# Optimization experiments

Hardware: AMD Instinct MI355X
Metric: run time of the kernel (lower is better)

Reference implementation:

```python
import jax, jax.numpy as jnp
import numpy as np

N, F, D, C, K, E, M = 50000, 512, 128, 128, 3, 20000, 8  # nodes, feat, emb, conv, cheb K, hyperedges, edge size
EPS = 1e-5


def setup_inputs() -> dict:
    key = jax.random.key(0)
    ks = jax.random.split(key, 9)
    pos_set = jax.random.normal(ks[0], (N, F), jnp.float32)
    # each hyperedge = M distinct nodes (contiguous window => distinct, like the original expansion assumes)
    base = jax.random.randint(ks[1], (E, 1), 0, N - M)
    members = (base + jnp.arange(M, dtype=jnp.int32)[None, :]).astype(jnp.int32)  # [E, M]
    # expansion(): full directed clique (no self loops) on the E*M duplicated entries
    row, col = np.where(~np.eye(M, dtype=bool))            # M*(M-1) intra-edge pairs
    offs = np.arange(E, dtype=np.int64)[:, None] * M
    edge_index = jnp.asarray(np.stack([(offs + row[None, :]).ravel(),
                                       (offs + col[None, :]).ravel()]), jnp.int32)  # [2, E*M*(M-1)]
    batch = jnp.asarray(np.repeat(np.arange(E, dtype=np.int64), M), jnp.int32)      # [E*M]
    W_enc = jax.random.normal(ks[2], (F, D), jnp.float32) / np.float32(np.sqrt(F))
    b_enc = jnp.zeros((D,), jnp.float32)
    gn_gamma = 1.0 + 0.1 * jax.random.normal(ks[3], (D,), jnp.float32)
    gn_beta = 0.01 * jax.random.normal(ks[4], (D,), jnp.float32)
    gn_alpha = 1.0 + 0.1 * jax.random.normal(ks[5], (D,), jnp.float32)
    cheb_W = jax.random.normal(ks[6], (K, D, C), jnp.float32) / np.float32(np.sqrt(D * K))
    cheb_b = jnp.zeros((C,), jnp.float32)
    lin_W = jax.random.normal(ks[7], (2 * C, 1), jnp.float32) / np.float32(np.sqrt(2 * C))
    lin_b = jnp.zeros((1,), jnp.float32)
    return dict(pos_set=pos_set, W_enc=W_enc, b_enc=b_enc, gn_gamma=gn_gamma, gn_beta=gn_beta,
                gn_alpha=gn_alpha, cheb_W=cheb_W, cheb_b=cheb_b, lin_W=lin_W, lin_b=lin_b,
                members=members, edge_index=edge_index, batch=batch)


def reference(pos_set, W_enc, b_enc, gn_gamma, gn_beta, gn_alpha, cheb_W, cheb_b,
              lin_W, lin_b, members, edge_index, batch):
    num_entries = E * M
    # running_type == 'structure': Hardtanh(Linear(feature))
    x = jnp.clip(pos_set @ W_enc + b_enc, -1.0, 1.0)                    # [N, D]
    # partition(): duplicate node features per (node, hyperedge) incidence
    xe = x[members.reshape(-1)]                                         # [E*M, D]
    # GraphNorm (per-hyperedge group): out = gamma*(x - alpha*mean)/sqrt(var+eps) + beta
    cnt = jax.ops.segment_sum(jnp.ones((num_entries,), xe.dtype), batch, num_segments=E)  # [E]
    mean = jax.ops.segment_sum(xe, batch, num_segments=E) / cnt[:, None]
    ctr = xe - gn_alpha * mean[batch]
    var = jax.ops.segment_sum(ctr * ctr, batch, num_segments=E) / cnt[:, None]
    xe = gn_gamma * ctr / jnp.sqrt(var + EPS)[batch] + gn_beta
    # AlphaDropout is identity at eval time
    # ChebConv: sym norm, lambda_max=2 => L_hat = -D^{-1/2} A D^{-1/2} (zero diagonal)
    src, dst = edge_index[0], edge_index[1]
    deg = jax.ops.segment_sum(jnp.ones_like(src, dtype=xe.dtype), dst, num_segments=num_entries)
    w = -jax.lax.rsqrt(deg[src] * deg[dst])                             # [nE] scaled-Laplacian weights

    def Lhat(h):  # sparse matvec via gather + segment scatter-add
        return jax.ops.segment_sum(w[:, None] * h[src], dst, num_segments=num_entries)

    Tx0 = xe
    Tx1 = Lhat(Tx0)
    out = Tx0 @ cheb_W[0] + Tx1 @ cheb_W[1]
    Tkm1, Tkm2 = Tx1, Tx0
    for k in range(2, K):  # K is a small static constant
        Tk = 2.0 * Lhat(Tkm1) - Tkm2
        out = out + Tk @ cheb_W[k]
        Tkm1, Tkm2 = Tk, Tkm1
    h = jnp.clip(out + cheb_b, -1.0, 1.0)                               # Hardtanh
    # poolings per hyperedge
    y_max = jax.ops.segment_max(h, batch, num_segments=E)
    y_min = jax.ops.segment_min(h, batch, num_segments=E)
    y_norm = jnp.sqrt(jax.ops.segment_sum(h * h, batch, num_segments=E) / cnt[:, None])
    y = jnp.concatenate([y_max - y_min, y_norm], axis=1)                # [E, 2C]
    logits = y @ lin_W + lin_b
    return jax.nn.sigmoid(logits).squeeze(-1)                           # [E] link probabilities
```

## Files before the change

### kernel.cpp

```cpp
#include <hip/hip_runtime.h>
#include <hip/hip_bf16.h>

#define NN   50000
#define FF   512
#define DD   128
#define CC   128
#define EE   20000
#define MM   8
#define EPSV 1e-5f

typedef __attribute__((ext_vector_type(8)))  short bfrag;
typedef __attribute__((ext_vector_type(16))) float f32x16;

#define MFMA32(a, b, c) __builtin_amdgcn_mfma_f32_32x32x16_bf16((a), (b), (c), 0, 0, 0)

__device__ __forceinline__ unsigned short f2bf(float f) {
    unsigned u = __builtin_bit_cast(unsigned, f);
    unsigned r = u + 0x7FFFu + ((u >> 16) & 1u);
    return (unsigned short)(r >> 16);
}
__device__ __forceinline__ float bf2f(unsigned short h) {
    unsigned u = ((unsigned)h) << 16;
    return __builtin_bit_cast(float, u);
}
__device__ __forceinline__ void split1(float a, short& hi, short& lo) {
    unsigned short h = f2bf(a);
    hi = (short)h;
    lo = (short)f2bf(a - bf2f(h));
}

__global__ void prep_kernel(const float* __restrict__ W_enc,
                            const float* __restrict__ cheb_W,
                            unsigned short* __restrict__ WencT_hi,
                            unsigned short* __restrict__ WencT_lo,
                            unsigned short* __restrict__ WabT_hi,
                            unsigned short* __restrict__ WabT_lo) {
    int tid = blockIdx.x * blockDim.x + threadIdx.x;
    int stride = gridDim.x * blockDim.x;
    for (int idx = tid; idx < DD * FF; idx += stride) {
        int n = idx / FF, k = idx % FF;
        float v = W_enc[k * DD + n];
        short hi, lo; split1(v, hi, lo);
        WencT_hi[idx] = (unsigned short)hi;
        WencT_lo[idx] = (unsigned short)lo;
    }
    const float c1 = 1.0f / 7.0f;
    const float c2 = -47.0f / 49.0f;
    const float c3 = -1.0f / 7.0f;
    const float c4 = 12.0f / 49.0f;
    for (int idx = tid; idx < DD * 256; idx += stride) {
        int c = idx / 256, k = idx % 256;
        float v;
        if (k < DD) {
            v = cheb_W[0 * DD * CC + k * CC + c]
              + c1 * cheb_W[1 * DD * CC + k * CC + c]
              + c2 * cheb_W[2 * DD * CC + k * CC + c];
        } else {
            int d = k - DD;
            v = c3 * cheb_W[1 * DD * CC + d * CC + c]
              + c4 * cheb_W[2 * DD * CC + d * CC + c];
        }
        short hi, lo; split1(v, hi, lo);
        WabT_hi[idx] = (unsigned short)hi;
        WabT_lo[idx] = (unsigned short)lo;
    }
}

__global__ __launch_bounds__(512, 6) void enc_kernel(
        const float* __restrict__ pos,
        const unsigned short* __restrict__ BT_hi,
        const unsigned short* __restrict__ BT_lo,
        const float* __restrict__ b_enc,
        float* __restrict__ x) {
    __shared__ unsigned short ahz[2][64 * 64];
    __shared__ unsigned short bhz[2][128 * 64];

    const int t = threadIdx.x;
    const int w = t >> 6, l = t & 63, l31 = l & 31, lg2 = l >> 5;
    const int wm = w & 1, wn = w >> 1;

    f32x16 acc;
#pragma unroll
    for (int i = 0; i < 16; i++) acc[i] = 0.f;

    for (int ph = 0; ph < 8; ph++) {
        if (ph) __syncthreads();
        {
            const int r = t >> 3, c8 = t & 7;
            int grow = blockIdx.x * 64 + r;
            if (grow >= NN) grow = NN - 1;
            const float* src = pos + (size_t)grow * FF + ph * 64 + c8 * 8;
            const float4 v0 = *(const float4*)src;
            const float4 v1 = *(const float4*)(src + 4);
            const float av[8] = {v0.x, v0.y, v0.z, v0.w, v1.x, v1.y, v1.z, v1.w};
            bfrag hi, lo;
#pragma unroll
            for (int j = 0; j < 8; j++) { short h, lo2; split1(av[j], h, lo2); hi[j] = h; lo[j] = lo2; }
            const int dst = r * 64 + ((c8 ^ (r & 7)) << 3);
            *(bfrag*)&ahz[0][dst] = hi;
            *(bfrag*)&ahz[1][dst] = lo;
        }
#pragma unroll
        for (int i = 0; i < 4; i++) {
            const int c = t + i * 512;
            const int arr = c >> 10, rc = c & 1023, n = rc >> 3, slot = rc & 7;
            const unsigned short* src = (arr ? BT_lo : BT_hi) + (size_t)n * FF + ph * 64 + slot * 8;
            *(bfrag*)&bhz[arr][n * 64 + ((slot ^ (n & 7)) << 3)] = *(const bfrag*)src;
        }
        __syncthreads();
#pragma unroll
        for (int ks = 0; ks < 4; ks++) {
            const int slot = ks * 2 + lg2;
            const int arow = wm * 32 + l31;
            const int aoff = arow * 64 + ((slot ^ (arow & 7)) << 3);
            const bfrag ahi = *(const bfrag*)&ahz[0][aoff];
            const bfrag alo = *(const bfrag*)&ahz[1][aoff];
            const int col = wn * 32 + l31;
            const int boff = col * 64 + ((slot ^ (col & 7)) << 3);
            const bfrag bhi = *(const bfrag*)&bhz[0][boff];
            const bfrag blo = *(const bfrag*)&bhz[1][boff];
            acc = MFMA32(ahi, bhi, acc);
            acc = MFMA32(ahi, blo, acc);
            acc = MFMA32(alo, bhi, acc);
        }
    }

    const int col = wn * 32 + l31;
    const float bias = b_enc[col];
    const int brow = blockIdx.x * 64 + wm * 32;
#pragma unroll
    for (int r = 0; r < 16; r++) {
        const int row = brow + (r & 3) + 8 * (r >> 2) + 4 * lg2;
        if (row < NN) {
            float v = acc[r] + bias;
            x[(size_t)row * DD + col] = fminf(1.0f, fmaxf(-1.0f, v));
        }
    }
}

__global__ __launch_bounds__(512, 4) void edge_kernel(
        const float* __restrict__ x,
        const int* __restrict__ members,
        const unsigned short* __restrict__ WabT_hi,
        const unsigned short* __restrict__ WabT_lo,
        const float* __restrict__ gn_gamma,
        const float* __restrict__ gn_beta,
        const float* __restrict__ gn_alpha,
        const float* __restrict__ cheb_b,
        const float* __restrict__ lin_W,
        const float* __restrict__ lin_b,
        float* __restrict__ out) {
    __shared__ unsigned short wa_hi[128 * 128];
    __shared__ unsigned short wb_hi[128 * 128];

    const int t = threadIdx.x;
    const int w = t >> 6, l = t & 63, l31 = l & 31, lg2 = l >> 5;

#pragma unroll
    for (int i = 0; i < 8; i++) {
        const int c = t + i * 512;
        const int arr = c >> 11, rc = c & 2047, col = rc >> 4, slot = rc & 15;
        const bfrag v = *(const bfrag*)(WabT_hi + (size_t)col * 256 + arr * 128 + slot * 8);
        unsigned short* dst = arr ? wb_hi : wa_hi;
        *(bfrag*)&dst[col * 128 + ((slot ^ (col & 15)) << 3)] = v;
    }

    const int node = members[blockIdx.x * 256 + w * 32 + l31];
    const float* xrow = x + (size_t)node * DD;

    __syncthreads();

    f32x16 acc[4];
#pragma unroll
    for (int nt = 0; nt < 4; nt++)
#pragma unroll
        for (int i = 0; i < 16; i++) acc[nt][i] = 0.f;

#pragma unroll
    for (int ks = 0; ks < 8; ks++) {
        const int koff = ks * 16 + lg2 * 8;
        const float4 a0 = *(const float4*)(xrow + koff);
        const float4 a1 = *(const float4*)(xrow + koff + 4);
        float v[8] = {a0.x, a0.y, a0.z, a0.w, a1.x, a1.y, a1.z, a1.w};
        float s[8];
#pragma unroll
        for (int j = 0; j < 8; j++) s[j] = v[j];
#pragma unroll
        for (int mk = 1; mk <= 4; mk <<= 1)
#pragma unroll
            for (int j = 0; j < 8; j++) s[j] += __shfl_xor(s[j], mk);

        {
            const float4 al0 = *(const float4*)(gn_alpha + koff);
            const float4 al1 = *(const float4*)(gn_alpha + koff + 4);
            const float al[8] = {al0.x, al0.y, al0.z, al0.w, al1.x, al1.y, al1.z, al1.w};
#pragma unroll
            for (int j = 0; j < 8; j++) {
                const float m = s[j] * 0.125f;
                v[j] = v[j] - al[j] * m;
                s[j] = m * (1.0f - al[j]);
            }
        }
        float t2[8];
#pragma unroll
        for (int j = 0; j < 8; j++) t2[j] = v[j] * v[j];
#pragma unroll
        for (int mk = 1; mk <= 4; mk <<= 1)
#pragma unroll
            for (int j = 0; j < 8; j++) t2[j] += __shfl_xor(t2[j], mk);

        bfrag ahi, alo, shi;
        {
            const float4 g0 = *(const float4*)(gn_gamma + koff);
            const float4 g1 = *(const float4*)(gn_gamma + koff + 4);
            const float4 b0 = *(const float4*)(gn_beta + koff);
            const float4 b1 = *(const float4*)(gn_beta + koff + 4);
            const float gm[8] = {g0.x, g0.y, g0.z, g0.w, g1.x, g1.y, g1.z, g1.w};
            const float bt[8] = {b0.x, b0.y, b0.z, b0.w, b1.x, b1.y, b1.z, b1.w};
#pragma unroll
            for (int j = 0; j < 8; j++) {
                const float sc = gm[j] * rsqrtf(t2[j] * 0.125f + EPSV);
                const float nv = sc * v[j] + bt[j];
                short h, lo2; split1(nv, h, lo2);
                ahi[j] = h; alo[j] = lo2;
                const float S = 8.0f * (sc * s[j] + bt[j]);
                shi[j] = (short)f2bf(S);
            }
        }

        const int slot = ks * 2 + lg2;
#pragma unroll
        for (int nt = 0; nt < 4; nt++) {
            const int col = nt * 32 + l31;
            const int woff = col * 128 + ((slot ^ (col & 15)) << 3);
            const bfrag wahi = *(const bfrag*)&wa_hi[woff];
            const bfrag wbh  = *(const bfrag*)&wb_hi[woff];
            const bfrag walo = *(const bfrag*)(WabT_lo + (size_t)col * 256 + koff);
            acc[nt] = MFMA32(ahi, wahi, acc[nt]);
            acc[nt] = MFMA32(ahi, walo, acc[nt]);
            acc[nt] = MFMA32(alo, wahi, acc[nt]);
            acc[nt] = MFMA32(shi, wbh,  acc[nt]);
        }
    }

    float p[4] = {0.f, 0.f, 0.f, 0.f};
#pragma unroll
    for (int nt = 0; nt < 4; nt++) {
        const int col = nt * 32 + l31;
        const float bias = cheb_b[col];
        const float w1 = lin_W[col], w2 = lin_W[DD + col];
#pragma unroll
        for (int e = 0; e < 4; e++) {
            float mx = -2.f, mn = 2.f, ssq = 0.f;
#pragma unroll
            for (int q = 0; q < 4; q++) {
                float h = acc[nt][e * 4 + q] + bias;
                h = fminf(1.0f, fmaxf(-1.0f, h));
                mx = fmaxf(mx, h); mn = fminf(mn, h); ssq += h * h;
            }
            mx = fmaxf(mx, __shfl_xor(mx, 32));
            mn = fminf(mn, __shfl_xor(mn, 32));
            ssq += __shfl_xor(ssq, 32);
            p[e] += (mx - mn) * w1 + sqrtf(ssq * 0.125f) * w2;
        }
    }
#pragma unroll
    for (int mk = 1; mk <= 16; mk <<= 1)
#pragma unroll
        for (int e = 0; e < 4; e++) p[e] += __shfl_xor(p[e], mk);
    if (l == 0) {
        const float b0 = lin_b[0];
#pragma unroll
        for (int e = 0; e < 4; e++) {
            const float z = p[e] + b0;
            out[blockIdx.x * 32 + w * 4 + e] = 1.0f / (1.0f + expf(-z));
        }
    }
}

extern "C" void kernel_launch(void* const* d_in, const int* in_sizes, int n_in,
                              void* d_out, int out_size, void* d_ws, size_t ws_size,
                              hipStream_t stream) {
    const float* pos    = (const float*)d_in[0];
    const float* W_enc  = (const float*)d_in[1];
    const float* b_enc  = (const float*)d_in[2];
    const float* gammaP = (const float*)d_in[3];
    const float* betaP  = (const float*)d_in[4];
    const float* alphaP = (const float*)d_in[5];
    const float* cheb_W = (const float*)d_in[6];
    const float* cheb_b = (const float*)d_in[7];
    const float* lin_W  = (const float*)d_in[8];
    const float* lin_b  = (const float*)d_in[9];
    const int*   members = (const int*)d_in[10];
    float* out = (float*)d_out;

    char* ws = (char*)d_ws;
    float* x = (float*)ws;
    unsigned short* WencT_hi = (unsigned short*)(ws + 25600000);
    unsigned short* WencT_lo = WencT_hi + DD * FF;
    unsigned short* WabT_hi  = WencT_lo + DD * FF;
    unsigned short* WabT_lo  = WabT_hi + DD * 256;

    prep_kernel<<<256, 256, 0, stream>>>(W_enc, cheb_W, WencT_hi, WencT_lo, WabT_hi, WabT_lo);
    enc_kernel<<<(NN + 63) / 64, 512, 0, stream>>>(pos, WencT_hi, WencT_lo, b_enc, x);
    edge_kernel<<<EE / 32, 512, 0, stream>>>(x, members, WabT_hi, WabT_lo,
                                             gammaP, betaP, alphaP, cheb_b, lin_W, lin_b, out);
}
```

Baseline: 262.5 us.

## Drop LDS staging; read pre-packed MFMA-fragment weights directly from global memory

```diff
diff --git a/kernel.cpp b/kernel.cpp
--- a/kernel.cpp
+++ b/kernel.cpp
@@ -31,118 +31,106 @@
 
 __global__ void prep_kernel(const float* __restrict__ W_enc,
                             const float* __restrict__ cheb_W,
-                            unsigned short* __restrict__ WencT_hi,
-                            unsigned short* __restrict__ WencT_lo,
-                            unsigned short* __restrict__ WabT_hi,
-                            unsigned short* __restrict__ WabT_lo) {
-    int tid = blockIdx.x * blockDim.x + threadIdx.x;
-    int stride = gridDim.x * blockDim.x;
-    for (int idx = tid; idx < DD * FF; idx += stride) {
-        int n = idx / FF, k = idx % FF;
-        float v = W_enc[k * DD + n];
-        short hi, lo; split1(v, hi, lo);
-        WencT_hi[idx] = (unsigned short)hi;
-        WencT_lo[idx] = (unsigned short)lo;
+                            unsigned short* __restrict__ Ep_hi,
+                            unsigned short* __restrict__ Ep_lo,
+                            unsigned short* __restrict__ Wp_hi,
+                            unsigned short* __restrict__ Wp_lo) {
+    const int tid = blockIdx.x * blockDim.x + threadIdx.x;
+    const int stride = gridDim.x * blockDim.x;
+    for (int p = tid; p < 64 * 128; p += stride) {
+        const int slot = p >> 7, n = p & 127;
+        bfrag fh, fl;
+#pragma unroll
+        for (int j = 0; j < 8; j++) {
+            const float v = W_enc[(size_t)(slot * 8 + j) * DD + n];
+            short h, lo; split1(v, h, lo);
+            fh[j] = h; fl[j] = lo;
+        }
+        *(bfrag*)&Ep_hi[(size_t)p * 8] = fh;
+        *(bfrag*)&Ep_lo[(size_t)p * 8] = fl;
     }
     const float c1 = 1.0f / 7.0f;
     const float c2 = -47.0f / 49.0f;
     const float c3 = -1.0f / 7.0f;
     const float c4 = 12.0f / 49.0f;
-    for (int idx = tid; idx < DD * 256; idx += stride) {
-        int c = idx / 256, k = idx % 256;
-        float v;
-        if (k < DD) {
-            v = cheb_W[0 * DD * CC + k * CC + c]
-              + c1 * cheb_W[1 * DD * CC + k * CC + c]
-              + c2 * cheb_W[2 * DD * CC + k * CC + c];
-        } else {
-            int d = k - DD;
-            v = c3 * cheb_W[1 * DD * CC + d * CC + c]
-              + c4 * cheb_W[2 * DD * CC + d * CC + c];
-        }
-        short hi, lo; split1(v, hi, lo);
-        WabT_hi[idx] = (unsigned short)hi;
-        WabT_lo[idx] = (unsigned short)lo;
-    }
-}
-
-__global__ __launch_bounds__(512, 6) void enc_kernel(
+    for (int p = tid; p < 32 * 128; p += stride) {
+        const int slot = p >> 7, c = p & 127;
+        bfrag fh, fl;
+#pragma unroll
+        for (int j = 0; j < 8; j++) {
+            const int k = slot * 8 + j;
+            float v;
+            if (k < DD) {
+                v = cheb_W[0 * DD * CC + k * CC + c]
+                  + c1 * cheb_W[1 * DD * CC + k * CC + c]
+                  + c2 * cheb_W[2 * DD * CC + k * CC + c];
+            } else {
+                const int d = k - DD;
+                v = c3 * cheb_W[1 * DD * CC + d * CC + c]
+                  + c4 * cheb_W[2 * DD * CC + d * CC + c];
+            }
+            short h, lo; split1(v, h, lo);
+            fh[j] = h; fl[j] = lo;
+        }
+        *(bfrag*)&Wp_hi[(size_t)p * 8] = fh;
+        *(bfrag*)&Wp_lo[(size_t)p * 8] = fl;
+    }
+}
+
+__global__ __launch_bounds__(256, 8) void enc_kernel(
         const float* __restrict__ pos,
-        const unsigned short* __restrict__ BT_hi,
-        const unsigned short* __restrict__ BT_lo,
+        const unsigned short* __restrict__ Ep_hi,
+        const unsigned short* __restrict__ Ep_lo,
         const float* __restrict__ b_enc,
         float* __restrict__ x) {
-    __shared__ unsigned short ahz[2][64 * 64];
-    __shared__ unsigned short bhz[2][128 * 64];
-
     const int t = threadIdx.x;
     const int w = t >> 6, l = t & 63, l31 = l & 31, lg2 = l >> 5;
-    const int wm = w & 1, wn = w >> 1;
+
+    int arow = blockIdx.x * 32 + l31;
+    if (arow >= NN) arow = NN - 1;
+    const float* aBase = pos + (size_t)arow * FF;
 
     f32x16 acc;
 #pragma unroll
     for (int i = 0; i < 16; i++) acc[i] = 0.f;
 
-    for (int ph = 0; ph < 8; ph++) {
-        if (ph) __syncthreads();
-        {
-            const int r = t >> 3, c8 = t & 7;
-            int grow = blockIdx.x * 64 + r;
-            if (grow >= NN) grow = NN - 1;
-            const float* src = pos + (size_t)grow * FF + ph * 64 + c8 * 8;
-            const float4 v0 = *(const float4*)src;
-            const float4 v1 = *(const float4*)(src + 4);
-            const float av[8] = {v0.x, v0.y, v0.z, v0.w, v1.x, v1.y, v1.z, v1.w};
-            bfrag hi, lo;
-#pragma unroll
-            for (int j = 0; j < 8; j++) { short h, lo2; split1(av[j], h, lo2); hi[j] = h; lo[j] = lo2; }
-            const int dst = r * 64 + ((c8 ^ (r & 7)) << 3);
-            *(bfrag*)&ahz[0][dst] = hi;
-            *(bfrag*)&ahz[1][dst] = lo;
-        }
-#pragma unroll
-        for (int i = 0; i < 4; i++) {
-            const int c = t + i * 512;
-            const int arr = c >> 10, rc = c & 1023, n = rc >> 3, slot = rc & 7;
-            const unsigned short* src = (arr ? BT_lo : BT_hi) + (size_t)n * FF + ph * 64 + slot * 8;
-            *(bfrag*)&bhz[arr][n * 64 + ((slot ^ (n & 7)) << 3)] = *(const bfrag*)src;
-        }
-        __syncthreads();
-#pragma unroll
-        for (int ks = 0; ks < 4; ks++) {
-            const int slot = ks * 2 + lg2;
-            const int arow = wm * 32 + l31;
-            const int aoff = arow * 64 + ((slot ^ (arow & 7)) << 3);
-            const bfrag ahi = *(const bfrag*)&ahz[0][aoff];
-            const bfrag alo = *(const bfrag*)&ahz[1][aoff];
-            const int col = wn * 32 + l31;
-            const int boff = col * 64 + ((slot ^ (col & 7)) << 3);
-            const bfrag bhi = *(const bfrag*)&bhz[0][boff];
-            const bfrag blo = *(const bfrag*)&bhz[1][boff];
-            acc = MFMA32(ahi, bhi, acc);
-            acc = MFMA32(ahi, blo, acc);
-            acc = MFMA32(alo, bhi, acc);
-        }
-    }
-
-    const int col = wn * 32 + l31;
+#pragma unroll 4
+    for (int ks = 0; ks < 32; ks++) {
+        const int koff = ks * 16 + lg2 * 8;
+        const float4 a0 = *(const float4*)(aBase + koff);
+        const float4 a1 = *(const float4*)(aBase + koff + 4);
+        const float av[8] = {a0.x, a0.y, a0.z, a0.w, a1.x, a1.y, a1.z, a1.w};
+        bfrag ahi, alo;
+#pragma unroll
+        for (int j = 0; j < 8; j++) { short h, lo2; split1(av[j], h, lo2); ahi[j] = h; alo[j] = lo2; }
+
+        const int slot = ks * 2 + lg2;
+        const size_t boff = ((size_t)slot * 128 + w * 32 + l31) * 8;
+        const bfrag bhi = *(const bfrag*)(Ep_hi + boff);
+        const bfrag blo = *(const bfrag*)(Ep_lo + boff);
+        acc = MFMA32(ahi, bhi, acc);
+        acc = MFMA32(ahi, blo, acc);
+        acc = MFMA32(alo, bhi, acc);
+    }
+
+    const int col = w * 32 + l31;
     const float bias = b_enc[col];
-    const int brow = blockIdx.x * 64 + wm * 32;
+    const int brow = blockIdx.x * 32;
 #pragma unroll
     for (int r = 0; r < 16; r++) {
         const int row = brow + (r & 3) + 8 * (r >> 2) + 4 * lg2;
         if (row < NN) {
-            float v = acc[r] + bias;
+            const float v = acc[r] + bias;
             x[(size_t)row * DD + col] = fminf(1.0f, fmaxf(-1.0f, v));
         }
     }
 }
 
-__global__ __launch_bounds__(512, 4) void edge_kernel(
+__global__ __launch_bounds__(256, 8) void edge_kernel(
         const float* __restrict__ x,
         const int* __restrict__ members,
-        const unsigned short* __restrict__ WabT_hi,
-        const unsigned short* __restrict__ WabT_lo,
+        const unsigned short* __restrict__ Wp_hi,
+        const unsigned short* __restrict__ Wp_lo,
         const float* __restrict__ gn_gamma,
         const float* __restrict__ gn_beta,
         const float* __restrict__ gn_alpha,
@@ -150,25 +138,11 @@
         const float* __restrict__ lin_W,
         const float* __restrict__ lin_b,
         float* __restrict__ out) {
-    __shared__ unsigned short wa_hi[128 * 128];
-    __shared__ unsigned short wb_hi[128 * 128];
-
     const int t = threadIdx.x;
     const int w = t >> 6, l = t & 63, l31 = l & 31, lg2 = l >> 5;
 
-#pragma unroll
-    for (int i = 0; i < 8; i++) {
-        const int c = t + i * 512;
-        const int arr = c >> 11, rc = c & 2047, col = rc >> 4, slot = rc & 15;
-        const bfrag v = *(const bfrag*)(WabT_hi + (size_t)col * 256 + arr * 128 + slot * 8);
-        unsigned short* dst = arr ? wb_hi : wa_hi;
-        *(bfrag*)&dst[col * 128 + ((slot ^ (col & 15)) << 3)] = v;
-    }
-
-    const int node = members[blockIdx.x * 256 + w * 32 + l31];
+    const int node = members[blockIdx.x * 128 + w * 32 + l31];
     const float* xrow = x + (size_t)node * DD;
-
-    __syncthreads();
 
     f32x16 acc[4];
 #pragma unroll
@@ -228,14 +202,16 @@
             }
         }
 
-        const int slot = ks * 2 + lg2;
+        const int slotN = ks * 2 + lg2;
+        const int slotS = 16 + slotN;
 #pragma unroll
         for (int nt = 0; nt < 4; nt++) {
             const int col = nt * 32 + l31;
-            const int woff = col * 128 + ((slot ^ (col & 15)) << 3);
-            const bfrag wahi = *(const bfrag*)&wa_hi[woff];
-            const bfrag wbh  = *(const bfrag*)&wb_hi[woff];
-            const bfrag walo = *(const bfrag*)(WabT_lo + (size_t)col * 256 + koff);
+            const size_t offN = ((size_t)slotN * 128 + col) * 8;
+            const size_t offS = ((size_t)slotS * 128 + col) * 8;
+            const bfrag wahi = *(const bfrag*)(Wp_hi + offN);
+            const bfrag walo = *(const bfrag*)(Wp_lo + offN);
+            const bfrag wbh  = *(const bfrag*)(Wp_hi + offS);
             acc[nt] = MFMA32(ahi, wahi, acc[nt]);
             acc[nt] = MFMA32(ahi, walo, acc[nt]);
             acc[nt] = MFMA32(alo, wahi, acc[nt]);
@@ -273,7 +249,7 @@
 #pragma unroll
         for (int e = 0; e < 4; e++) {
             const float z = p[e] + b0;
-            out[blockIdx.x * 32 + w * 4 + e] = 1.0f / (1.0f + expf(-z));
+            out[blockIdx.x * 16 + w * 4 + e] = 1.0f / (1.0f + expf(-z));
         }
     }
 }
@@ -296,13 +272,13 @@
 
     char* ws = (char*)d_ws;
     float* x = (float*)ws;
-    unsigned short* WencT_hi = (unsigned short*)(ws + 25600000);
-    unsigned short* WencT_lo = WencT_hi + DD * FF;
-    unsigned short* WabT_hi  = WencT_lo + DD * FF;
-    unsigned short* WabT_lo  = WabT_hi + DD * 256;
-
-    prep_kernel<<<256, 256, 0, stream>>>(W_enc, cheb_W, WencT_hi, WencT_lo, WabT_hi, WabT_lo);
-    enc_kernel<<<(NN + 63) / 64, 512, 0, stream>>>(pos, WencT_hi, WencT_lo, b_enc, x);
-    edge_kernel<<<EE / 32, 512, 0, stream>>>(x, members, WabT_hi, WabT_lo,
+    unsigned short* Ep_hi = (unsigned short*)(ws + 25600000);
+    unsigned short* Ep_lo = Ep_hi + 64 * 128 * 8;
+    unsigned short* Wp_hi = Ep_lo + 64 * 128 * 8;
+    unsigned short* Wp_lo = Wp_hi + 32 * 128 * 8;
+
+    prep_kernel<<<32, 256, 0, stream>>>(W_enc, cheb_W, Ep_hi, Ep_lo, Wp_hi, Wp_lo);
+    enc_kernel<<<(NN + 31) / 32, 256, 0, stream>>>(pos, Ep_hi, Ep_lo, b_enc, x);
+    edge_kernel<<<EE / 16, 256, 0, stream>>>(x, members, Wp_hi, Wp_lo,
                                              gammaP, betaP, alphaP, cheb_b, lin_W, lin_b, out);
 }
```

Result: slower. 431.8 us (+64.5%).
